# Optimization experiments

Measured on AMD Instinct MI355X. Metric: run time of the kernel, lower is better.

Reference implementation:

```python
import jax, jax.numpy as jnp
import numpy as np

B, S, D = 2, 1024, 1024
E = 8          # routed experts
I = 1024       # per-expert intermediate
IS = 1024      # shared expert intermediate
TOP_K = 2
NUM_SHARED = 1


def setup_inputs() -> dict:
    key = jax.random.key(0)
    ks = jax.random.split(key, 8)
    scale = 0.02
    return {
        "x": jax.random.normal(ks[0], (B, S, D), dtype=jnp.float32),
        "w_gate": jax.random.normal(ks[1], (D, E), dtype=jnp.float32) * scale,
        "wg": jax.random.normal(ks[2], (E, D, I), dtype=jnp.float32) * scale,  # expert gate_proj
        "wu": jax.random.normal(ks[3], (E, D, I), dtype=jnp.float32) * scale,  # expert up_proj
        "wd": jax.random.normal(ks[4], (E, I, D), dtype=jnp.float32) * scale,  # expert down_proj
        "ws_g": jax.random.normal(ks[5], (NUM_SHARED, D, IS), dtype=jnp.float32) * scale,
        "ws_u": jax.random.normal(ks[6], (NUM_SHARED, D, IS), dtype=jnp.float32) * scale,
        "ws_d": jax.random.normal(ks[7], (NUM_SHARED, IS, D), dtype=jnp.float32) * scale,
    }


def _swiglu(t, w_gate_proj, w_up, w_down):
    # t: [N, D]
    g = t @ w_gate_proj            # [N, I]
    u = t @ w_up                   # [N, I]
    return (jax.nn.silu(g) * u) @ w_down  # [N, D]


def reference(x, w_gate, wg, wu, wd, ws_g, ws_u, ws_d):
    Bb, Ss, Dd = x.shape
    x_flat = x.reshape(Bb * Ss, Dd)                  # [N, D]
    N = x_flat.shape[0]

    # --- router ---
    logits = x_flat @ w_gate                          # [N, E]
    topk_logits, topk_idx = jax.lax.top_k(logits, TOP_K)
    topk_w = jax.nn.softmax(topk_logits, axis=-1)     # [N, K]

    # --- aux load-balancing loss ---
    one_hot = jax.nn.one_hot(topk_idx, E, dtype=jnp.float32)  # [N, K, E]
    f = one_hot.sum(axis=1).mean(axis=0)                       # [E]
    P = jax.nn.softmax(logits, axis=-1).mean(axis=0)           # [E]
    aux_loss = E * jnp.sum(f * P)

    # --- combine weights: cw[n, e] = sum_k topk_w[n,k] * 1[topk_idx[n,k]==e] ---
    cw = jnp.einsum("nk,nke->ne", topk_w, one_hot)             # [N, E]

    # --- routed experts: dense compute over all experts, weighted combine ---
    g = jnp.einsum("nd,edi->eni", x_flat, wg)                  # [E, N, I]
    u = jnp.einsum("nd,edi->eni", x_flat, wu)                  # [E, N, I]
    a = jax.nn.silu(g) * u                                     # [E, N, I]
    y = jnp.einsum("eni,eid->end", a, wd)                      # [E, N, D]
    routed = jnp.einsum("ne,end->nd", cw, y)                   # [N, D]

    # --- shared experts ---
    shared = jnp.zeros_like(x_flat)
    for s in range(NUM_SHARED):
        shared = shared + _swiglu(x_flat, ws_g[s], ws_u[s], ws_d[s])

    out = (routed + shared).reshape(Bb, Ss, Dd)
    return out, aux_loss
```

## Files before the change

### kernel.cpp

```cpp
#include <hip/hip_runtime.h>
#include <math.h>

typedef unsigned short u16;
typedef __attribute__((ext_vector_type(8))) short short8;
typedef __attribute__((ext_vector_type(4))) float f32x4;
typedef __attribute__((ext_vector_type(4))) unsigned short u16x4;

#define N_TOK 2048
#define DIM 1024
#define OUT_ELEMS 2097152

#define GLDS16(gp, lp) __builtin_amdgcn_global_load_lds( \
    (const __attribute__((address_space(1))) unsigned int*)(gp), \
    (__attribute__((address_space(3))) unsigned int*)(lp), 16, 0, 0)

__device__ __forceinline__ u16 f2bf(float f) {
    union { float f; unsigned u; } v; v.f = f;
    unsigned r = (v.u + 0x7FFFu + ((v.u >> 16) & 1u)) >> 16;
    return (u16)r;
}

__global__ void k_init(int* __restrict__ tlist, int* __restrict__ curs) {
    int i = blockIdx.x * 256 + threadIdx.x;
    tlist[4096 + i] = i;
    if (i < 16) curs[i] = 0;
}

__global__ void k_cvt_x(const float* __restrict__ x, u16* __restrict__ xb) {
    int i = blockIdx.x * 256 + threadIdx.x;
    f32x4 v = ((const f32x4*)x)[i];
    u16x4 o;
    o.x = f2bf(v.x); o.y = f2bf(v.y); o.z = f2bf(v.z); o.w = f2bf(v.w);
    ((u16x4*)xb)[i] = o;
}

__global__ void k_cvt_w(const float* __restrict__ wg, const float* __restrict__ wu,
                        const float* __restrict__ wd, const float* __restrict__ wsg,
                        const float* __restrict__ wsu, const float* __restrict__ wsd,
                        u16* __restrict__ wgt, u16* __restrict__ wut,
                        u16* __restrict__ wdt, u16* __restrict__ wsgt,
                        u16* __restrict__ wsut, u16* __restrict__ wsdt) {
    __shared__ float tile[32][33];
    int bx = blockIdx.x;
    int mat = bx >> 10;
    int tl  = bx & 1023;
    int tr = tl >> 5, tc = tl & 31;
    const float* src; u16* dst;
    if      (mat <  8) { src = wg  + (size_t)mat * 1048576;        dst = wgt + (size_t)mat * 1048576; }
    else if (mat < 16) { src = wu  + (size_t)(mat - 8) * 1048576;  dst = wut + (size_t)(mat - 8) * 1048576; }
    else if (mat < 24) { src = wd  + (size_t)(mat - 16) * 1048576; dst = wdt + (size_t)(mat - 16) * 1048576; }
    else if (mat == 24){ src = wsg; dst = wsgt; }
    else if (mat == 25){ src = wsu; dst = wsut; }
    else               { src = wsd; dst = wsdt; }
    int tx = threadIdx.x & 31, ty = threadIdx.x >> 5;
#pragma unroll
    for (int j = 0; j < 4; j++)
        tile[ty + j * 8][tx] = src[(size_t)(tr * 32 + ty + j * 8) * 1024 + tc * 32 + tx];
    __syncthreads();
    int row = threadIdx.x >> 3;
    int c4  = threadIdx.x & 7;
    u16x4 o;
    o.x = f2bf(tile[c4 * 4 + 0][row]);
    o.y = f2bf(tile[c4 * 4 + 1][row]);
    o.z = f2bf(tile[c4 * 4 + 2][row]);
    o.w = f2bf(tile[c4 * 4 + 3][row]);
    *(u16x4*)(dst + (size_t)(tc * 32 + row) * 1024 + tr * 32 + c4 * 4) = o;
}

__global__ void k_router(const float* __restrict__ x, const float* __restrict__ wgate,
                         float* __restrict__ Ptok, int* __restrict__ tidx,
                         float* __restrict__ tw) {
    int wave = threadIdx.x >> 6;
    int lane = threadIdx.x & 63;
    int n = blockIdx.x * 4 + wave;
    const float* xr = x + (size_t)n * DIM;
    float acc[8] = {0.f,0.f,0.f,0.f,0.f,0.f,0.f,0.f};
    for (int d = lane; d < DIM; d += 64) {
        float xv = xr[d];
        const float* wr = wgate + d * 8;
#pragma unroll
        for (int e = 0; e < 8; e++) acc[e] += xv * wr[e];
    }
#pragma unroll
    for (int off = 32; off; off >>= 1) {
#pragma unroll
        for (int e = 0; e < 8; e++) acc[e] += __shfl_xor(acc[e], off);
    }
    if (lane == 0) {
        float mx = acc[0];
#pragma unroll
        for (int e = 1; e < 8; e++) mx = fmaxf(mx, acc[e]);
        float p[8], s = 0.f;
#pragma unroll
        for (int e = 0; e < 8; e++) { p[e] = expf(acc[e] - mx); s += p[e]; }
        float inv = 1.f / s;
#pragma unroll
        for (int e = 0; e < 8; e++) Ptok[n * 8 + e] = p[e] * inv;
        int i0 = 0; float b0 = acc[0];
#pragma unroll
        for (int e = 1; e < 8; e++) if (acc[e] > b0) { b0 = acc[e]; i0 = e; }
        int i1 = -1; float b1 = -3.4e38f;
#pragma unroll
        for (int e = 0; e < 8; e++) if (e != i0 && acc[e] > b1) { b1 = acc[e]; i1 = e; }
        float w0 = 1.f / (1.f + expf(b1 - b0));
        tidx[n * 2] = i0; tidx[n * 2 + 1] = i1;
        tw[n * 2] = w0;   tw[n * 2 + 1] = 1.f - w0;
    }
}

__global__ void k_reduce(const float* __restrict__ Ptok, const int* __restrict__ tidx,
                         float* __restrict__ out, int* __restrict__ counts,
                         int* __restrict__ offs) {
    __shared__ float ps[256][8];
    __shared__ int cnt[8];
    int t = threadIdx.x;
    if (t < 8) cnt[t] = 0;
    __syncthreads();
    float p[8] = {0.f,0.f,0.f,0.f,0.f,0.f,0.f,0.f};
    for (int n = t; n < N_TOK; n += 256) {
#pragma unroll
        for (int e = 0; e < 8; e++) p[e] += Ptok[n * 8 + e];
        atomicAdd(&cnt[tidx[n * 2]], 1);
        atomicAdd(&cnt[tidx[n * 2 + 1]], 1);
    }
#pragma unroll
    for (int e = 0; e < 8; e++) ps[t][e] = p[e];
    __syncthreads();
    for (int off = 128; off; off >>= 1) {
        if (t < off) {
#pragma unroll
            for (int e = 0; e < 8; e++) ps[t][e] += ps[t + off][e];
        }
        __syncthreads();
    }
    if (t == 0) {
        float aux = 0.f;
        for (int e = 0; e < 8; e++)
            aux += ((float)cnt[e] / (float)N_TOK) * (ps[0][e] / (float)N_TOK);
        out[OUT_ELEMS] = 8.f * aux;
        int o = 0;
        for (int e = 0; e < 8; e++) { offs[e] = o; counts[e] = cnt[e]; o += cnt[e]; }
        offs[8] = 4096; counts[8] = 2048;
    }
}

__global__ void k_scatter(const int* __restrict__ tidx, const int* __restrict__ offs,
                          int* __restrict__ curs, int* __restrict__ tlist,
                          int* __restrict__ slots) {
    int n = blockIdx.x * 256 + threadIdx.x;
    if (n >= N_TOK) return;
#pragma unroll
    for (int k = 0; k < 2; k++) {
        int e = tidx[n * 2 + k];
        int p = atomicAdd(&curs[e], 1);
        int sl = offs[e] + p;
        tlist[sl] = n;
        slots[n * 2 + k] = sl;
    }
}

__global__ __launch_bounds__(256, 2)
void k_gemm1(const u16* __restrict__ xb, const u16* __restrict__ wgt,
             const u16* __restrict__ wut, const u16* __restrict__ wsgt,
             const u16* __restrict__ wsut, const int* __restrict__ tlist,
             const int* __restrict__ counts, const int* __restrict__ offs,
             u16* __restrict__ H) {
    int bx = blockIdx.x;
    int job = bx >> 7;
    int mt = (bx >> 3) & 15;
    int nt = bx & 7;
    int jcnt = counts[job];
    int m0 = mt << 7;
    if (m0 >= jcnt) return;
    int joff = offs[job];
    int n0 = nt << 7;
    const u16* Bg = (job < 8) ? (wgt + (size_t)job * 1048576) : wsgt;
    const u16* Bu = (job < 8) ? (wut + (size_t)job * 1048576) : wsut;

    __shared__ __attribute__((aligned(128))) u16 As[4096];
    __shared__ __attribute__((aligned(128))) u16 Bgs[4096];
    __shared__ __attribute__((aligned(128))) u16 Bus[4096];

    int t = threadIdx.x;
    int wave = t >> 6, lane = t & 63;
    int ch = (lane & 3) * 8;
    int r0 = (wave * 2 + 0) * 16 + (lane >> 2);
    int r1 = (wave * 2 + 1) * 16 + (lane >> 2);
    int tok0 = tlist[joff + m0 + r0];
    int tok1 = tlist[joff + m0 + r1];
    const u16* a0 = xb + (size_t)tok0 * 1024 + ch;
    const u16* a1 = xb + (size_t)tok1 * 1024 + ch;
    const u16* g0 = Bg + (size_t)(n0 + r0) * 1024 + ch;
    const u16* g1 = Bg + (size_t)(n0 + r1) * 1024 + ch;
    const u16* u0 = Bu + (size_t)(n0 + r0) * 1024 + ch;
    const u16* u1 = Bu + (size_t)(n0 + r1) * 1024 + ch;
    u16* lA0 = As  + (wave * 2 + 0) * 512;  u16* lA1 = As  + (wave * 2 + 1) * 512;
    u16* lG0 = Bgs + (wave * 2 + 0) * 512;  u16* lG1 = Bgs + (wave * 2 + 1) * 512;
    u16* lU0 = Bus + (wave * 2 + 0) * 512;  u16* lU1 = Bus + (wave * 2 + 1) * 512;

    int wm = (wave >> 1) << 6, wn = (wave & 1) << 6;
    int quad = lane >> 4, lr = lane & 15;

    f32x4 accg[4][4], accu[4][4];
    f32x4 zz = {0.f, 0.f, 0.f, 0.f};
#pragma unroll
    for (int i = 0; i < 4; i++)
#pragma unroll
        for (int j = 0; j < 4; j++) { accg[i][j] = zz; accu[i][j] = zz; }

    for (int k0 = 0; k0 < 1024; k0 += 32) {
        GLDS16(a0 + k0, lA0);  GLDS16(a1 + k0, lA1);
        GLDS16(g0 + k0, lG0);  GLDS16(g1 + k0, lG1);
        GLDS16(u0 + k0, lU0);  GLDS16(u1 + k0, lU1);
        __syncthreads();
        short8 af[4], bgf[4], buf[4];
#pragma unroll
        for (int i = 0; i < 4; i++) {
            af[i]  = *(const short8*)(As  + (wm + i * 16 + lr) * 32 + quad * 8);
            bgf[i] = *(const short8*)(Bgs + (wn + i * 16 + lr) * 32 + quad * 8);
            buf[i] = *(const short8*)(Bus + (wn + i * 16 + lr) * 32 + quad * 8);
        }
#pragma unroll
        for (int mi = 0; mi < 4; mi++)
#pragma unroll
            for (int ni = 0; ni < 4; ni++) {
                accg[mi][ni] = __builtin_amdgcn_mfma_f32_16x16x32_bf16(af[mi], bgf[ni], accg[mi][ni], 0, 0, 0);
                accu[mi][ni] = __builtin_amdgcn_mfma_f32_16x16x32_bf16(af[mi], buf[ni], accu[mi][ni], 0, 0, 0);
            }
        __syncthreads();
    }
#pragma unroll
    for (int mi = 0; mi < 4; mi++) {
        int rowb = m0 + wm + mi * 16 + quad * 4;
#pragma unroll
        for (int rr = 0; rr < 4; rr++) {
            int row = rowb + rr;
            if (row < jcnt) {
                size_t base = (size_t)(joff + row) * 1024 + n0 + wn;
#pragma unroll
                for (int ni = 0; ni < 4; ni++) {
                    float g = accg[mi][ni][rr];
                    float u = accu[mi][ni][rr];
                    float h = (g / (1.f + expf(-g))) * u;
                    H[base + ni * 16 + lr] = f2bf(h);
                }
            }
        }
    }
}

__global__ __launch_bounds__(256, 2)
void k_gemm2(const u16* __restrict__ H, const u16* __restrict__ wdt,
             const u16* __restrict__ wsdt, const int* __restrict__ counts,
             const int* __restrict__ offs, float* __restrict__ Y) {
    int bx = blockIdx.x;
    int job = bx >> 7;
    int mt = (bx >> 3) & 15;
    int nt = bx & 7;
    int jcnt = counts[job];
    int m0 = mt << 7;
    if (m0 >= jcnt) return;
    int joff = offs[job];
    int n0 = nt << 7;
    const u16* Bt = (job < 8) ? (wdt + (size_t)job * 1048576) : wsdt;

    __shared__ __attribute__((aligned(128))) u16 As[4096];
    __shared__ __attribute__((aligned(128))) u16 Bs[4096];

    int t = threadIdx.x;
    int wave = t >> 6, lane = t & 63;
    int ch = (lane & 3) * 8;
    int r0 = (wave * 2 + 0) * 16 + (lane >> 2);
    int r1 = (wave * 2 + 1) * 16 + (lane >> 2);
    const u16* a0 = H + (size_t)(joff + m0 + r0) * 1024 + ch;
    const u16* a1 = H + (size_t)(joff + m0 + r1) * 1024 + ch;
    const u16* b0 = Bt + (size_t)(n0 + r0) * 1024 + ch;
    const u16* b1 = Bt + (size_t)(n0 + r1) * 1024 + ch;
    u16* lA0 = As + (wave * 2 + 0) * 512;  u16* lA1 = As + (wave * 2 + 1) * 512;
    u16* lB0 = Bs + (wave * 2 + 0) * 512;  u16* lB1 = Bs + (wave * 2 + 1) * 512;

    int wm = (wave >> 1) << 6, wn = (wave & 1) << 6;
    int quad = lane >> 4, lr = lane & 15;

    f32x4 acc[4][4];
    f32x4 zz = {0.f, 0.f, 0.f, 0.f};
#pragma unroll
    for (int i = 0; i < 4; i++)
#pragma unroll
        for (int j = 0; j < 4; j++) acc[i][j] = zz;

    for (int k0 = 0; k0 < 1024; k0 += 32) {
        GLDS16(a0 + k0, lA0);  GLDS16(a1 + k0, lA1);
        GLDS16(b0 + k0, lB0);  GLDS16(b1 + k0, lB1);
        __syncthreads();
        short8 af[4], bf[4];
#pragma unroll
        for (int i = 0; i < 4; i++) {
            af[i] = *(const short8*)(As + (wm + i * 16 + lr) * 32 + quad * 8);
            bf[i] = *(const short8*)(Bs + (wn + i * 16 + lr) * 32 + quad * 8);
        }
#pragma unroll
        for (int mi = 0; mi < 4; mi++)
#pragma unroll
            for (int ni = 0; ni < 4; ni++)
                acc[mi][ni] = __builtin_amdgcn_mfma_f32_16x16x32_bf16(af[mi], bf[ni], acc[mi][ni], 0, 0, 0);
        __syncthreads();
    }
#pragma unroll
    for (int mi = 0; mi < 4; mi++) {
        int rowb = m0 + wm + mi * 16 + quad * 4;
#pragma unroll
        for (int rr = 0; rr < 4; rr++) {
            int row = rowb + rr;
            if (row < jcnt) {
                float* yrow = Y + (size_t)(joff + row) * 1024 + n0 + wn;
#pragma unroll
                for (int ni = 0; ni < 4; ni++)
                    yrow[ni * 16 + lr] = acc[mi][ni][rr];
            }
        }
    }
}

__global__ void k_combine(const float* __restrict__ Y, const int* __restrict__ slots,
                          const float* __restrict__ tw, float* __restrict__ out) {
    int n = blockIdx.x;
    int d = threadIdx.x;
    int s0 = slots[n * 2], s1 = slots[n * 2 + 1];
    float w0 = tw[n * 2], w1 = tw[n * 2 + 1];
    f32x4 y0 = ((const f32x4*)(Y + (size_t)s0 * 1024))[d];
    f32x4 y1 = ((const f32x4*)(Y + (size_t)s1 * 1024))[d];
    f32x4 ys = ((const f32x4*)(Y + (size_t)(4096 + n) * 1024))[d];
    f32x4 r;
    r.x = w0 * y0.x + w1 * y1.x + ys.x;
    r.y = w0 * y0.y + w1 * y1.y + ys.y;
    r.z = w0 * y0.z + w1 * y1.z + ys.z;
    r.w = w0 * y0.w + w1 * y1.w + ys.w;
    ((f32x4*)(out + (size_t)n * 1024))[d] = r;
}

extern "C" void kernel_launch(void* const* d_in, const int* in_sizes, int n_in,
                              void* d_out, int out_size, void* d_ws, size_t ws_size,
                              hipStream_t stream) {
    const float* x     = (const float*)d_in[0];
    const float* wgate = (const float*)d_in[1];
    const float* wg    = (const float*)d_in[2];
    const float* wu    = (const float*)d_in[3];
    const float* wd    = (const float*)d_in[4];
    const float* wsg   = (const float*)d_in[5];
    const float* wsu   = (const float*)d_in[6];
    const float* wsd   = (const float*)d_in[7];
    float* out = (float*)d_out;

    char* ws = (char*)d_ws;
    u16*   xb    = (u16*)(ws + 0);
    u16*   wgt   = (u16*)(ws + 4194304);
    u16*   wut   = (u16*)(ws + 20971520);
    u16*   wdt   = (u16*)(ws + 37748736);
    u16*   wsgt  = (u16*)(ws + 54525952);
    u16*   wsut  = (u16*)(ws + 56623104);
    u16*   wsdt  = (u16*)(ws + 58720256);
    u16*   H     = (u16*)(ws + 60817408);
    float* Y     = (float*)(ws + 4194304);
    float* Ptok  = (float*)(ws + 73400320);
    int*   tidx  = (int*)(ws + 73465856);
    float* tw    = (float*)(ws + 73482240);
    int*   tlist = (int*)(ws + 73498624);
    int*   slots = (int*)(ws + 73523200);
    int*   counts= (int*)(ws + 73539584);
    int*   offs  = (int*)(ws + 73539648);
    int*   curs  = (int*)(ws + 73539712);

    k_init<<<8, 256, 0, stream>>>(tlist, curs);
    k_cvt_x<<<2048, 256, 0, stream>>>(x, xb);
    k_cvt_w<<<27648, 256, 0, stream>>>(wg, wu, wd, wsg, wsu, wsd,
                                       wgt, wut, wdt, wsgt, wsut, wsdt);
    k_router<<<512, 256, 0, stream>>>(x, wgate, Ptok, tidx, tw);
    k_reduce<<<1, 256, 0, stream>>>(Ptok, tidx, out, counts, offs);
    k_scatter<<<8, 256, 0, stream>>>(tidx, offs, curs, tlist, slots);
    k_gemm1<<<1152, 256, 0, stream>>>(xb, wgt, wut, wsgt, wsut, tlist, counts, offs, H);
    k_gemm2<<<1152, 256, 0, stream>>>(H, wdt, wsdt, counts, offs, Y);
    k_combine<<<2048, 256, 0, stream>>>(Y, slots, tw, out);
}
```

Before: 284.6 us.

## Widen weight transpose tiles, fuse router reductions, store expert outputs as bf16

The weight transpose-convert kernel now uses 64x64 tiles with float4 loads and 8-wide bf16 stores, which cuts the block count and gives wider memory transactions. The separate single-block reduce kernel is replaced by per-block shared atomics in the router plus global atomics and a tiny finalize kernel, and the per-token probability buffer is dropped. Expert outputs Y are written as bf16 instead of fp32, halving the traffic in gemm2 stores and combine loads at some cost in precision. The cvt_w launch is also moved after the routing kernels.

```diff
diff --git a/kernel.cpp b/kernel.cpp
--- a/kernel.cpp
+++ b/kernel.cpp
@@ -5,6 +5,7 @@
 typedef __attribute__((ext_vector_type(8))) short short8;
 typedef __attribute__((ext_vector_type(4))) float f32x4;
 typedef __attribute__((ext_vector_type(4))) unsigned short u16x4;
+typedef __attribute__((ext_vector_type(8))) unsigned short u16x8;
 
 #define N_TOK 2048
 #define DIM 1024
@@ -19,11 +20,17 @@
     unsigned r = (v.u + 0x7FFFu + ((v.u >> 16) & 1u)) >> 16;
     return (u16)r;
 }
-
-__global__ void k_init(int* __restrict__ tlist, int* __restrict__ curs) {
+__device__ __forceinline__ float bf2f(u16 h) {
+    union { unsigned u; float f; } v; v.u = ((unsigned)h) << 16;
+    return v.f;
+}
+
+__global__ void k_init(int* __restrict__ tlist, int* __restrict__ curs,
+                       float* __restrict__ Psum, int* __restrict__ cnt8) {
     int i = blockIdx.x * 256 + threadIdx.x;
     tlist[4096 + i] = i;
     if (i < 16) curs[i] = 0;
+    if (i < 8) { Psum[i] = 0.f; cnt8[i] = 0; }
 }
 
 __global__ void k_cvt_x(const float* __restrict__ x, u16* __restrict__ xb) {
@@ -40,11 +47,11 @@
                         u16* __restrict__ wgt, u16* __restrict__ wut,
                         u16* __restrict__ wdt, u16* __restrict__ wsgt,
                         u16* __restrict__ wsut, u16* __restrict__ wsdt) {
-    __shared__ float tile[32][33];
+    __shared__ float tile[64 * 68];
     int bx = blockIdx.x;
-    int mat = bx >> 10;
-    int tl  = bx & 1023;
-    int tr = tl >> 5, tc = tl & 31;
+    int mat = bx >> 8;
+    int tl  = bx & 255;
+    int tr = tl >> 4, tc = tl & 15;
     const float* src; u16* dst;
     if      (mat <  8) { src = wg  + (size_t)mat * 1048576;        dst = wgt + (size_t)mat * 1048576; }
     else if (mat < 16) { src = wu  + (size_t)(mat - 8) * 1048576;  dst = wut + (size_t)(mat - 8) * 1048576; }
@@ -52,26 +59,38 @@
     else if (mat == 24){ src = wsg; dst = wsgt; }
     else if (mat == 25){ src = wsu; dst = wsut; }
     else               { src = wsd; dst = wsdt; }
-    int tx = threadIdx.x & 31, ty = threadIdx.x >> 5;
-#pragma unroll
-    for (int j = 0; j < 4; j++)
-        tile[ty + j * 8][tx] = src[(size_t)(tr * 32 + ty + j * 8) * 1024 + tc * 32 + tx];
+    int t = threadIdx.x;
+    int col = (t & 15) * 4;
+    int rbase = t >> 4;
+#pragma unroll
+    for (int j = 0; j < 4; j++) {
+        int row = rbase + j * 16;
+        f32x4 v = *(const f32x4*)(src + (size_t)(tr * 64 + row) * 1024 + tc * 64 + col);
+        *(f32x4*)(tile + row * 68 + col) = v;
+    }
     __syncthreads();
-    int row = threadIdx.x >> 3;
-    int c4  = threadIdx.x & 7;
-    u16x4 o;
-    o.x = f2bf(tile[c4 * 4 + 0][row]);
-    o.y = f2bf(tile[c4 * 4 + 1][row]);
-    o.z = f2bf(tile[c4 * 4 + 2][row]);
-    o.w = f2bf(tile[c4 * 4 + 3][row]);
-    *(u16x4*)(dst + (size_t)(tc * 32 + row) * 1024 + tr * 32 + c4 * 4) = o;
+    int oc = t & 63;
+    int q  = t >> 6;
+#pragma unroll
+    for (int j = 0; j < 2; j++) {
+        int kb = q * 8 + j * 32;
+        u16x8 o;
+#pragma unroll
+        for (int i = 0; i < 8; i++) o[i] = f2bf(tile[(kb + i) * 68 + oc]);
+        *(u16x8*)(dst + (size_t)(tc * 64 + oc) * 1024 + tr * 64 + kb) = o;
+    }
 }
 
 __global__ void k_router(const float* __restrict__ x, const float* __restrict__ wgate,
-                         float* __restrict__ Ptok, int* __restrict__ tidx,
-                         float* __restrict__ tw) {
-    int wave = threadIdx.x >> 6;
-    int lane = threadIdx.x & 63;
+                         int* __restrict__ tidx, float* __restrict__ tw,
+                         float* __restrict__ Psum, int* __restrict__ cnt8) {
+    __shared__ float sP[8];
+    __shared__ int   sC[8];
+    int t = threadIdx.x;
+    if (t < 8) { sP[t] = 0.f; sC[t] = 0; }
+    __syncthreads();
+    int wave = t >> 6;
+    int lane = t & 63;
     int n = blockIdx.x * 4 + wave;
     const float* xr = x + (size_t)n * DIM;
     float acc[8] = {0.f,0.f,0.f,0.f,0.f,0.f,0.f,0.f};
@@ -95,7 +114,7 @@
         for (int e = 0; e < 8; e++) { p[e] = expf(acc[e] - mx); s += p[e]; }
         float inv = 1.f / s;
 #pragma unroll
-        for (int e = 0; e < 8; e++) Ptok[n * 8 + e] = p[e] * inv;
+        for (int e = 0; e < 8; e++) atomicAdd(&sP[e], p[e] * inv);
         int i0 = 0; float b0 = acc[0];
 #pragma unroll
         for (int e = 1; e < 8; e++) if (acc[e] > b0) { b0 = acc[e]; i0 = e; }
@@ -105,41 +124,28 @@
         float w0 = 1.f / (1.f + expf(b1 - b0));
         tidx[n * 2] = i0; tidx[n * 2 + 1] = i1;
         tw[n * 2] = w0;   tw[n * 2 + 1] = 1.f - w0;
-    }
-}
-
-__global__ void k_reduce(const float* __restrict__ Ptok, const int* __restrict__ tidx,
-                         float* __restrict__ out, int* __restrict__ counts,
-                         int* __restrict__ offs) {
-    __shared__ float ps[256][8];
-    __shared__ int cnt[8];
-    int t = threadIdx.x;
-    if (t < 8) cnt[t] = 0;
+        atomicAdd(&sC[i0], 1);
+        atomicAdd(&sC[i1], 1);
+    }
     __syncthreads();
-    float p[8] = {0.f,0.f,0.f,0.f,0.f,0.f,0.f,0.f};
-    for (int n = t; n < N_TOK; n += 256) {
-#pragma unroll
-        for (int e = 0; e < 8; e++) p[e] += Ptok[n * 8 + e];
-        atomicAdd(&cnt[tidx[n * 2]], 1);
-        atomicAdd(&cnt[tidx[n * 2 + 1]], 1);
-    }
-#pragma unroll
-    for (int e = 0; e < 8; e++) ps[t][e] = p[e];
-    __syncthreads();
-    for (int off = 128; off; off >>= 1) {
-        if (t < off) {
-#pragma unroll
-            for (int e = 0; e < 8; e++) ps[t][e] += ps[t + off][e];
-        }
-        __syncthreads();
-    }
-    if (t == 0) {
+    if (t < 8) {
+        atomicAdd(&Psum[t], sP[t]);
+        atomicAdd(&cnt8[t], sC[t]);
+    }
+}
+
+__global__ void k_finalize(const float* __restrict__ Psum, const int* __restrict__ cnt8,
+                           float* __restrict__ out, int* __restrict__ counts,
+                           int* __restrict__ offs) {
+    if (threadIdx.x == 0) {
         float aux = 0.f;
-        for (int e = 0; e < 8; e++)
-            aux += ((float)cnt[e] / (float)N_TOK) * (ps[0][e] / (float)N_TOK);
-        out[OUT_ELEMS] = 8.f * aux;
         int o = 0;
-        for (int e = 0; e < 8; e++) { offs[e] = o; counts[e] = cnt[e]; o += cnt[e]; }
+        for (int e = 0; e < 8; e++) {
+            int c = cnt8[e];
+            aux += (float)c * Psum[e];
+            offs[e] = o; counts[e] = c; o += c;
+        }
+        out[OUT_ELEMS] = 8.f * aux / ((float)N_TOK * (float)N_TOK);
         offs[8] = 4096; counts[8] = 2048;
     }
 }
@@ -252,7 +258,7 @@
 __global__ __launch_bounds__(256, 2)
 void k_gemm2(const u16* __restrict__ H, const u16* __restrict__ wdt,
              const u16* __restrict__ wsdt, const int* __restrict__ counts,
-             const int* __restrict__ offs, float* __restrict__ Y) {
+             const int* __restrict__ offs, u16* __restrict__ Y) {
     int bx = blockIdx.x;
     int job = bx >> 7;
     int mt = (bx >> 3) & 15;
@@ -313,29 +319,29 @@
         for (int rr = 0; rr < 4; rr++) {
             int row = rowb + rr;
             if (row < jcnt) {
-                float* yrow = Y + (size_t)(joff + row) * 1024 + n0 + wn;
+                u16* yrow = Y + (size_t)(joff + row) * 1024 + n0 + wn;
 #pragma unroll
                 for (int ni = 0; ni < 4; ni++)
-                    yrow[ni * 16 + lr] = acc[mi][ni][rr];
+                    yrow[ni * 16 + lr] = f2bf(acc[mi][ni][rr]);
             }
         }
     }
 }
 
-__global__ void k_combine(const float* __restrict__ Y, const int* __restrict__ slots,
+__global__ void k_combine(const u16* __restrict__ Y, const int* __restrict__ slots,
                           const float* __restrict__ tw, float* __restrict__ out) {
     int n = blockIdx.x;
     int d = threadIdx.x;
     int s0 = slots[n * 2], s1 = slots[n * 2 + 1];
     float w0 = tw[n * 2], w1 = tw[n * 2 + 1];
-    f32x4 y0 = ((const f32x4*)(Y + (size_t)s0 * 1024))[d];
-    f32x4 y1 = ((const f32x4*)(Y + (size_t)s1 * 1024))[d];
-    f32x4 ys = ((const f32x4*)(Y + (size_t)(4096 + n) * 1024))[d];
+    u16x4 y0 = ((const u16x4*)(Y + (size_t)s0 * 1024))[d];
+    u16x4 y1 = ((const u16x4*)(Y + (size_t)s1 * 1024))[d];
+    u16x4 ys = ((const u16x4*)(Y + (size_t)(4096 + n) * 1024))[d];
     f32x4 r;
-    r.x = w0 * y0.x + w1 * y1.x + ys.x;
-    r.y = w0 * y0.y + w1 * y1.y + ys.y;
-    r.z = w0 * y0.z + w1 * y1.z + ys.z;
-    r.w = w0 * y0.w + w1 * y1.w + ys.w;
+    r.x = w0 * bf2f(y0.x) + w1 * bf2f(y1.x) + bf2f(ys.x);
+    r.y = w0 * bf2f(y0.y) + w1 * bf2f(y1.y) + bf2f(ys.y);
+    r.z = w0 * bf2f(y0.z) + w1 * bf2f(y1.z) + bf2f(ys.z);
+    r.w = w0 * bf2f(y0.w) + w1 * bf2f(y1.w) + bf2f(ys.w);
     ((f32x4*)(out + (size_t)n * 1024))[d] = r;
 }
 
@@ -361,23 +367,24 @@
     u16*   wsut  = (u16*)(ws + 56623104);
     u16*   wsdt  = (u16*)(ws + 58720256);
     u16*   H     = (u16*)(ws + 60817408);
-    float* Y     = (float*)(ws + 4194304);
-    float* Ptok  = (float*)(ws + 73400320);
-    int*   tidx  = (int*)(ws + 73465856);
-    float* tw    = (float*)(ws + 73482240);
-    int*   tlist = (int*)(ws + 73498624);
-    int*   slots = (int*)(ws + 73523200);
-    int*   counts= (int*)(ws + 73539584);
-    int*   offs  = (int*)(ws + 73539648);
-    int*   curs  = (int*)(ws + 73539712);
-
-    k_init<<<8, 256, 0, stream>>>(tlist, curs);
+    u16*   Y     = (u16*)(ws + 4194304);
+    int*   tidx  = (int*)(ws + 73400320);
+    float* tw    = (float*)(ws + 73416704);
+    int*   tlist = (int*)(ws + 73433088);
+    int*   slots = (int*)(ws + 73457664);
+    int*   counts= (int*)(ws + 73474048);
+    int*   offs  = (int*)(ws + 73474112);
+    int*   curs  = (int*)(ws + 73474176);
+    float* Psum  = (float*)(ws + 73474240);
+    int*   cnt8  = (int*)(ws + 73474304);
+
+    k_init<<<8, 256, 0, stream>>>(tlist, curs, Psum, cnt8);
     k_cvt_x<<<2048, 256, 0, stream>>>(x, xb);
-    k_cvt_w<<<27648, 256, 0, stream>>>(wg, wu, wd, wsg, wsu, wsd,
-                                       wgt, wut, wdt, wsgt, wsut, wsdt);
-    k_router<<<512, 256, 0, stream>>>(x, wgate, Ptok, tidx, tw);
-    k_reduce<<<1, 256, 0, stream>>>(Ptok, tidx, out, counts, offs);
+    k_router<<<512, 256, 0, stream>>>(x, wgate, tidx, tw, Psum, cnt8);
+    k_finalize<<<1, 64, 0, stream>>>(Psum, cnt8, out, counts, offs);
     k_scatter<<<8, 256, 0, stream>>>(tidx, offs, curs, tlist, slots);
+    k_cvt_w<<<6912, 256, 0, stream>>>(wg, wu, wd, wsg, wsu, wsd,
+                                      wgt, wut, wdt, wsgt, wsut, wsdt);
     k_gemm1<<<1152, 256, 0, stream>>>(xb, wgt, wut, wsgt, wsut, tlist, counts, offs, H);
     k_gemm2<<<1152, 256, 0, stream>>>(H, wdt, wsdt, counts, offs, Y);
     k_combine<<<2048, 256, 0, stream>>>(Y, slots, tw, out);
```

Result: no change. 288.8 us (+1.5%).
